# Kernel tuning notes

Hardware: AMD Instinct MI355X
Metric: run time of the kernel (lower is better)

The kernel has to match this reference:

```python
import jax, jax.numpy as jnp
import numpy as np

B, IN, H = 16384, 1024, 1024


def setup_inputs() -> dict:
    key = jax.random.key(0)
    ks = jax.random.split(key, 16)
    stdv = 1.0 / np.sqrt(H)
    u = lambda k, shape: jax.random.uniform(k, shape, jnp.float32, -stdv, stdv)
    return {
        "input": jax.random.normal(ks[0], (B, IN), jnp.float32),
        "prev_h": jax.random.normal(ks[1], (B, H), jnp.float32),
        "prev_c": jax.random.normal(ks[2], (B, H), jnp.float32),
        "weight_xi": u(ks[3], (IN, H)), "weight_hi": u(ks[4], (H, H)),
        "weight_xf": u(ks[5], (IN, H)), "weight_hf": u(ks[6], (H, H)),
        "weight_xu": u(ks[7], (IN, H)), "weight_hu": u(ks[8], (H, H)),
        "weight_xo": u(ks[9], (IN, H)), "weight_ho": u(ks[10], (H, H)),
        "bias_i": u(ks[11], (H,)), "bias_f": u(ks[12], (H,)),
        "bias_o": u(ks[13], (H,)), "bias_u": u(ks[14], (H,)),
    }


def reference(input, prev_h, prev_c,
              weight_xi, weight_hi, weight_xf, weight_hf,
              weight_xu, weight_hu, weight_xo, weight_ho,
              bias_i, bias_f, bias_o, bias_u):
    i = jax.nn.sigmoid(input @ weight_xi + prev_h @ weight_hi + bias_i)
    f = jax.nn.sigmoid(input @ weight_xf + prev_h @ weight_hf + bias_f)
    o = jax.nn.sigmoid(input @ weight_xo + prev_h @ weight_ho + bias_o)
    u = jnp.tanh(input @ weight_xu + prev_h @ weight_hu + bias_u)
    c = f * prev_c + i * u
    h = o * jnp.tanh(c)
    return (h, c)
```

## Files before the change

kernel.cpp:

```cpp
#include <hip/hip_runtime.h>
#include <hip/hip_bf16.h>
#include <stdint.h>
#include <type_traits>


typedef short bf16x8 __attribute__((ext_vector_type(8)));
typedef unsigned short u16x8 __attribute__((ext_vector_type(8)));
typedef float f32x16 __attribute__((ext_vector_type(16)));

__device__ __forceinline__ unsigned short f2bf(float f) {
    union { float f; uint32_t u; } v; v.f = f;
    uint32_t r = v.u + 0x7FFFu + ((v.u >> 16) & 1u);
    return (unsigned short)(r >> 16);
}

__device__ __forceinline__ float fsig(float x) { return 1.0f / (1.0f + __expf(-x)); }
__device__ __forceinline__ float ftanh(float x) { return 2.0f * fsig(2.0f * x) - 1.0f; }

__global__ __launch_bounds__(256) void pack_a_kernel(const float* __restrict__ input,
                                                     const float* __restrict__ prev_h,
                                                     unsigned short* __restrict__ Apk) {
    long idx = (long)blockIdx.x * 256 + threadIdx.x;
    long e0 = idx * 8;
    int b = (int)(e0 >> 11);
    int k = (int)(e0 & 2047);
    const float* src = (k < 1024) ? (input + (size_t)b * 1024 + k)
                                  : (prev_h + (size_t)b * 1024 + (k - 1024));
    float4 lo = *(const float4*)src;
    float4 hi = *(const float4*)(src + 4);
    u16x8 o;
    o[0] = f2bf(lo.x); o[1] = f2bf(lo.y); o[2] = f2bf(lo.z); o[3] = f2bf(lo.w);
    o[4] = f2bf(hi.x); o[5] = f2bf(hi.y); o[6] = f2bf(hi.z); o[7] = f2bf(hi.w);
    *(u16x8*)(Apk + e0) = o;
}

__global__ __launch_bounds__(256) void pack_b_kernel(
        const float* __restrict__ wxi, const float* __restrict__ wxf,
        const float* __restrict__ wxo, const float* __restrict__ wxu,
        const float* __restrict__ whi, const float* __restrict__ whf,
        const float* __restrict__ who, const float* __restrict__ whu,
        unsigned short* __restrict__ Bpk) {
    int idx = blockIdx.x * 256 + threadIdx.x;
    int g  = idx >> 18;
    int r  = idx & 262143;
    int kc = r >> 10;
    int j  = r & 1023;
    const float* wx = (g == 0) ? wxi : (g == 1) ? wxf : (g == 2) ? wxo : wxu;
    const float* wh = (g == 0) ? whi : (g == 1) ? whf : (g == 2) ? who : whu;
    int k0 = kc * 8;
    const float* src = (k0 < 1024) ? (wx + (size_t)k0 * 1024 + j)
                                   : (wh + (size_t)(k0 - 1024) * 1024 + j);
    u16x8 o;
#pragma unroll
    for (int t = 0; t < 8; ++t) o[t] = f2bf(src[(size_t)t * 1024]);
    *(u16x8*)(Bpk + (((size_t)(g * 1024 + j)) << 11) + k0) = o;
}


#define GLL(gp, lp) __builtin_amdgcn_global_load_lds( \
        (__attribute__((address_space(1))) void*)(gp), \
        (__attribute__((address_space(3))) void*)(lp), 16, 0, 0)

#define BAR() do { asm volatile("" ::: "memory"); __builtin_amdgcn_s_barrier(); \
                   asm volatile("" ::: "memory"); } while (0)

__global__ __launch_bounds__(512, 2) void lstm_gemm_kernel(
        const unsigned short* __restrict__ Apk,
        const unsigned short* __restrict__ Bpk,
        const float* __restrict__ prev_c,
        const float* __restrict__ bi, const float* __restrict__ bf_,
        const float* __restrict__ bo, const float* __restrict__ bu,
        float* __restrict__ out_h, float* __restrict__ out_c) {
    __shared__ __align__(16) unsigned char smem[131072];
    const int tid = threadIdx.x;
    const int w = tid >> 6, l = tid & 63;
    const int l31 = l & 31, l5 = l >> 5;
    const int wr = w >> 1, wc = w & 1;

    const int bid = blockIdx.x;
    const int sw = ((bid & 7) << 7) + (bid >> 3);
    const int tileRow = sw & 63, tileCol = sw >> 6;
    const int rowBase = tileRow * 256;
    const int jBase = tileCol * 64;

    const int key = (l31 >> 1) & 3;
    int aoff[2][2], boff[4][2];
#pragma unroll
    for (int m = 0; m < 2; ++m)
#pragma unroll
        for (int ks = 0; ks < 2; ++ks)
            aoff[m][ks] = (wr * 64 + m * 32 + l31) * 64 + ((ks * 2 + l5) ^ key) * 16;
#pragma unroll
    for (int g = 0; g < 4; ++g)
#pragma unroll
        for (int ks = 0; ks < 2; ++ks)
            boff[g][ks] = 16384 + (g * 64 + wc * 32 + l31) * 64 + ((ks * 2 + l5) ^ key) * 16;

    const int rloc = tid >> 2;
    const int sigS = ((l & 3) ^ ((l >> 3) & 3)) * 8;
    const unsigned short* aS0 = Apk + (size_t)(rowBase +   0 + rloc) * 2048 + sigS;
    const unsigned short* aS1 = Apk + (size_t)(rowBase + 128 + rloc) * 2048 + sigS;
    const unsigned short* bS0 = Bpk + (((size_t)(((rloc >> 6) + 0) * 1024 + jBase + (rloc & 63))) << 11) + sigS;
    const unsigned short* bS1 = Bpk + (((size_t)(((rloc >> 6) + 2) * 1024 + jBase + (rloc & 63))) << 11) + sigS;
    const int wB = w * 1024;

#define STAGE4(T) do { const int _bb = ((T) & 3) * 32768; \
        GLL(aS0 + (size_t)(T) * 32, smem + _bb +     0 + wB); \
        GLL(aS1 + (size_t)(T) * 32, smem + _bb +  8192 + wB); \
        GLL(bS0 + (size_t)(T) * 32, smem + _bb + 16384 + wB); \
        GLL(bS1 + (size_t)(T) * 32, smem + _bb + 24576 + wB); } while (0)

    f32x16 acc[2][4];
#pragma unroll
    for (int m = 0; m < 2; ++m)
#pragma unroll
        for (int g = 0; g < 4; ++g)
#pragma unroll
            for (int q = 0; q < 16; ++q) acc[m][g][q] = 0.f;

    bf16x8 aE[4], bE[8], aO[4], bO[8];

    auto ldfr = [&](int t, bf16x8 (&da)[4], bf16x8 (&db)[8]) {
        const int bt = (t & 3) * 32768;
#pragma unroll
        for (int m = 0; m < 2; ++m)
#pragma unroll
            for (int ks = 0; ks < 2; ++ks)
                da[m * 2 + ks] = *(const bf16x8*)(smem + bt + aoff[m][ks]);
#pragma unroll
        for (int g = 0; g < 4; ++g)
#pragma unroll
            for (int ks = 0; ks < 2; ++ks)
                db[g * 2 + ks] = *(const bf16x8*)(smem + bt + boff[g][ks]);
    };

    STAGE4(0); STAGE4(1); STAGE4(2);
    asm volatile("s_waitcnt vmcnt(4)" ::: "memory");
    BAR();
    ldfr(0, aE, bE);

    auto slice = [&](int t, auto vnc, auto stgc, auto nxtc,
                     bf16x8 (&ca)[4], bf16x8 (&cb)[8],
                     bf16x8 (&na)[4], bf16x8 (&nb)[8]) {
        constexpr int VN = decltype(vnc)::value;
        constexpr bool STG = decltype(stgc)::value;
        constexpr bool NXT = decltype(nxtc)::value;
        if constexpr (STG) STAGE4(t + 3);
        if constexpr (NXT) ldfr(t + 1, na, nb);
#pragma unroll
        for (int ks = 0; ks < 2; ++ks)
#pragma unroll
            for (int m = 0; m < 2; ++m)
#pragma unroll
                for (int g = 0; g < 4; ++g)
                    acc[m][g] = __builtin_amdgcn_mfma_f32_32x32x16_bf16(
                        ca[m * 2 + ks], cb[g * 2 + ks], acc[m][g], 0, 0, 0);
        if constexpr (VN == 4)      asm volatile("s_waitcnt vmcnt(4)" ::: "memory");
        else if constexpr (VN == 0) asm volatile("s_waitcnt vmcnt(0)" ::: "memory");
        if constexpr (VN >= 0) BAR();
    };

    using c4 = std::integral_constant<int, 4>;
    using c0 = std::integral_constant<int, 0>;
    using cm = std::integral_constant<int, -1>;
    using bT = std::integral_constant<bool, true>;
    using bF = std::integral_constant<bool, false>;

#pragma unroll 1
    for (int t = 0; t < 60; t += 2) {
        slice(t,     c4{}, bT{}, bT{}, aE, bE, aO, bO);
        slice(t + 1, c4{}, bT{}, bT{}, aO, bO, aE, bE);
    }
    slice(60, c4{}, bT{}, bT{}, aE, bE, aO, bO);
    slice(61, c0{}, bF{}, bT{}, aO, bO, aE, bE);
    slice(62, cm{}, bF{}, bT{}, aE, bE, aO, bO);
    slice(63, cm{}, bF{}, bF{}, aO, bO, aE, bE);

    const int colIdx = jBase + wc * 32 + l31;
    const float vbi = bi[colIdx], vbf = bf_[colIdx], vbo = bo[colIdx], vbu = bu[colIdx];
    const int rowB = rowBase + wr * 64 + 4 * l5;
#pragma unroll
    for (int m = 0; m < 2; ++m) {
#pragma unroll
        for (int q = 0; q < 16; ++q) {
            const int row = rowB + m * 32 + (q & 3) + 8 * (q >> 2);
            const size_t idx = (size_t)row * 1024 + colIdx;
            float zi = acc[m][0][q] + vbi;
            float zf = acc[m][1][q] + vbf;
            float zo = acc[m][2][q] + vbo;
            float zu = acc[m][3][q] + vbu;
            float iv = fsig(zi), fv = fsig(zf), ov = fsig(zo), uv = ftanh(zu);
            float cv = fv * prev_c[idx] + iv * uv;
            out_c[idx] = cv;
            out_h[idx] = ov * ftanh(cv);
        }
    }
#undef STAGE4
}

extern "C" void kernel_launch(void* const* d_in, const int* in_sizes, int n_in,
                              void* d_out, int out_size, void* d_ws, size_t ws_size,
                              hipStream_t stream) {
    const float* input  = (const float*)d_in[0];
    const float* prev_h = (const float*)d_in[1];
    const float* prev_c = (const float*)d_in[2];
    const float* wxi = (const float*)d_in[3];
    const float* whi = (const float*)d_in[4];
    const float* wxf = (const float*)d_in[5];
    const float* whf = (const float*)d_in[6];
    const float* wxu = (const float*)d_in[7];
    const float* whu = (const float*)d_in[8];
    const float* wxo = (const float*)d_in[9];
    const float* who = (const float*)d_in[10];
    const float* bi  = (const float*)d_in[11];
    const float* bf_ = (const float*)d_in[12];
    const float* bo  = (const float*)d_in[13];
    const float* bu  = (const float*)d_in[14];

    unsigned short* Apk = (unsigned short*)d_ws;
    unsigned short* Bpk = (unsigned short*)((char*)d_ws + (size_t)67108864);

    float* out_h = (float*)d_out;
    float* out_c = out_h + (size_t)16384 * 1024;

    pack_a_kernel<<<dim3(16384), dim3(256), 0, stream>>>(input, prev_h, Apk);
    pack_b_kernel<<<dim3(4096), dim3(256), 0, stream>>>(wxi, wxf, wxo, wxu,
                                                        whi, whf, who, whu, Bpk);
    lstm_gemm_kernel<<<dim3(1024), dim3(512), 0, stream>>>(Apk, Bpk, prev_c,
                                                           bi, bf_, bo, bu, out_h, out_c);
}
```

Before: 360.2 us.

## Restructure LDS layout to MFMA-native order and simplify pipeline depth

Changes global-to-LDS staging so each wave loads rows in the exact fragment order MFMA reads, removing the XOR swizzle. Register double-buffering of fragments is dropped: each slice now loads its fragments from LDS right before the MFMAs. Global prefetch distance is reduced from three stages ahead to two. This simplifies addressing and lowers register pressure, but removes the overlap of LDS reads with MFMAs and may cause LDS bank conflicts without the swizzle.

```diff
diff --git a/kernel.cpp b/kernel.cpp
--- a/kernel.cpp
+++ b/kernel.cpp
@@ -83,32 +83,32 @@
     const int rowBase = tileRow * 256;
     const int jBase = tileCol * 64;
 
-    const int key = (l31 >> 1) & 3;
     int aoff[2][2], boff[4][2];
 #pragma unroll
     for (int m = 0; m < 2; ++m)
 #pragma unroll
         for (int ks = 0; ks < 2; ++ks)
-            aoff[m][ks] = (wr * 64 + m * 32 + l31) * 64 + ((ks * 2 + l5) ^ key) * 16;
+            aoff[m][ks] = (wr * 2 + m) * 2048 + (ks * 2 + l5) * 512 + l31 * 16;
 #pragma unroll
     for (int g = 0; g < 4; ++g)
 #pragma unroll
         for (int ks = 0; ks < 2; ++ks)
-            boff[g][ks] = 16384 + (g * 64 + wc * 32 + l31) * 64 + ((ks * 2 + l5) ^ key) * 16;
-
-    const int rloc = tid >> 2;
-    const int sigS = ((l & 3) ^ ((l >> 3) & 3)) * 8;
-    const unsigned short* aS0 = Apk + (size_t)(rowBase +   0 + rloc) * 2048 + sigS;
-    const unsigned short* aS1 = Apk + (size_t)(rowBase + 128 + rloc) * 2048 + sigS;
-    const unsigned short* bS0 = Bpk + (((size_t)(((rloc >> 6) + 0) * 1024 + jBase + (rloc & 63))) << 11) + sigS;
-    const unsigned short* bS1 = Bpk + (((size_t)(((rloc >> 6) + 2) * 1024 + jBase + (rloc & 63))) << 11) + sigS;
-    const int wB = w * 1024;
+            boff[g][ks] = 16384 + g * 4096 + wc * 2048 + (ks * 2 + l5) * 512 + l31 * 16;
+
+    const unsigned short* aSq0 = Apk + (size_t)(rowBase + w * 32 + l31) * 2048 + (0 * 2 + l5) * 8;
+    const unsigned short* aSq1 = Apk + (size_t)(rowBase + w * 32 + l31) * 2048 + (1 * 2 + l5) * 8;
+    const size_t bRow = (size_t)((w >> 1) * 1024 + jBase + (w & 1) * 32 + l31) << 11;
+    const unsigned short* bSq0 = Bpk + bRow + (0 * 2 + l5) * 8;
+    const unsigned short* bSq1 = Bpk + bRow + (1 * 2 + l5) * 8;
+    const int aD0 = w * 2048, aD1 = w * 2048 + 1024;
+    const int bD0 = 16384 + (w >> 1) * 4096 + (w & 1) * 2048;
+    const int bD1 = bD0 + 1024;
 
 #define STAGE4(T) do { const int _bb = ((T) & 3) * 32768; \
-        GLL(aS0 + (size_t)(T) * 32, smem + _bb +     0 + wB); \
-        GLL(aS1 + (size_t)(T) * 32, smem + _bb +  8192 + wB); \
-        GLL(bS0 + (size_t)(T) * 32, smem + _bb + 16384 + wB); \
-        GLL(bS1 + (size_t)(T) * 32, smem + _bb + 24576 + wB); } while (0)
+        GLL(aSq0 + (size_t)(T) * 32, smem + _bb + aD0); \
+        GLL(aSq1 + (size_t)(T) * 32, smem + _bb + aD1); \
+        GLL(bSq0 + (size_t)(T) * 32, smem + _bb + bD0); \
+        GLL(bSq1 + (size_t)(T) * 32, smem + _bb + bD1); } while (0)
 
     f32x16 acc[2][4];
 #pragma unroll
@@ -118,35 +118,26 @@
 #pragma unroll
             for (int q = 0; q < 16; ++q) acc[m][g][q] = 0.f;
 
-    bf16x8 aE[4], bE[8], aO[4], bO[8];
-
-    auto ldfr = [&](int t, bf16x8 (&da)[4], bf16x8 (&db)[8]) {
-        const int bt = (t & 3) * 32768;
-#pragma unroll
-        for (int m = 0; m < 2; ++m)
-#pragma unroll
-            for (int ks = 0; ks < 2; ++ks)
-                da[m * 2 + ks] = *(const bf16x8*)(smem + bt + aoff[m][ks]);
-#pragma unroll
-        for (int g = 0; g < 4; ++g)
-#pragma unroll
-            for (int ks = 0; ks < 2; ++ks)
-                db[g * 2 + ks] = *(const bf16x8*)(smem + bt + boff[g][ks]);
-    };
-
-    STAGE4(0); STAGE4(1); STAGE4(2);
+    STAGE4(0); STAGE4(1);
     asm volatile("s_waitcnt vmcnt(4)" ::: "memory");
     BAR();
-    ldfr(0, aE, bE);
-
-    auto slice = [&](int t, auto vnc, auto stgc, auto nxtc,
-                     bf16x8 (&ca)[4], bf16x8 (&cb)[8],
-                     bf16x8 (&na)[4], bf16x8 (&nb)[8]) {
+
+    auto slice = [&](int t, auto vnc, auto stgc) {
         constexpr int VN = decltype(vnc)::value;
         constexpr bool STG = decltype(stgc)::value;
-        constexpr bool NXT = decltype(nxtc)::value;
-        if constexpr (STG) STAGE4(t + 3);
-        if constexpr (NXT) ldfr(t + 1, na, nb);
+        const int bt = (t & 3) * 32768;
+        if constexpr (STG) STAGE4(t + 2);
+        bf16x8 av[2][2], bv[4][2];
+#pragma unroll
+        for (int m = 0; m < 2; ++m)
+#pragma unroll
+            for (int ks = 0; ks < 2; ++ks)
+                av[m][ks] = *(const bf16x8*)(smem + bt + aoff[m][ks]);
+#pragma unroll
+        for (int g = 0; g < 4; ++g)
+#pragma unroll
+            for (int ks = 0; ks < 2; ++ks)
+                bv[g][ks] = *(const bf16x8*)(smem + bt + boff[g][ks]);
 #pragma unroll
         for (int ks = 0; ks < 2; ++ks)
 #pragma unroll
@@ -154,7 +145,7 @@
 #pragma unroll
                 for (int g = 0; g < 4; ++g)
                     acc[m][g] = __builtin_amdgcn_mfma_f32_32x32x16_bf16(
-                        ca[m * 2 + ks], cb[g * 2 + ks], acc[m][g], 0, 0, 0);
+                        av[m][ks], bv[g][ks], acc[m][g], 0, 0, 0);
         if constexpr (VN == 4)      asm volatile("s_waitcnt vmcnt(4)" ::: "memory");
         else if constexpr (VN == 0) asm volatile("s_waitcnt vmcnt(0)" ::: "memory");
         if constexpr (VN >= 0) BAR();
@@ -167,14 +158,9 @@
     using bF = std::integral_constant<bool, false>;
 
 #pragma unroll 1
-    for (int t = 0; t < 60; t += 2) {
-        slice(t,     c4{}, bT{}, bT{}, aE, bE, aO, bO);
-        slice(t + 1, c4{}, bT{}, bT{}, aO, bO, aE, bE);
-    }
-    slice(60, c4{}, bT{}, bT{}, aE, bE, aO, bO);
-    slice(61, c0{}, bF{}, bT{}, aO, bO, aE, bE);
-    slice(62, cm{}, bF{}, bT{}, aE, bE, aO, bO);
-    slice(63, cm{}, bF{}, bF{}, aO, bO, aE, bE);
+    for (int t = 0; t < 62; ++t) slice(t, c4{}, bT{});
+    slice(62, c0{}, bF{});
+    slice(63, cm{}, bF{});
 
     const int colIdx = jBase + wc * 32 + l31;
     const float vbi = bi[colIdx], vbf = bf_[colIdx], vbo = bo[colIdx], vbu = bu[colIdx];
```

Measured after the change: 403.8 us. +12.1%, slower.
